# Performance work log

Measured on AMD Instinct MI355X. Metric: run time of the kernel, lower is better.

Reference implementation:

```python
import jax, jax.numpy as jnp
import numpy as np

N, C, T, V = 32, 128, 256, 25
K = 5  # temporal kernel size; reflect-pad 2*(K-1)//2 = 4 rows on top
EPS = 1e-5


def _inorm(x):
    # InstanceNorm2d(affine=False): normalize each (n,c) plane over (T,V)
    m = jnp.mean(x, axis=(2, 3), keepdims=True)
    v = jnp.var(x, axis=(2, 3), keepdims=True)
    return (x - m) * jax.lax.rsqrt(v + EPS)


def setup_inputs() -> dict:
    key = jax.random.key(0)
    ks = jax.random.split(key, 5)
    x = jax.random.normal(ks[0], (N, C, T, V), jnp.float32)
    PA = jax.random.normal(ks[1], (V, V), jnp.float32)          # learned adjacency
    Wd = jax.random.normal(ks[2], (C, C), jnp.float32) * 0.05    # 1x1 conv weight (O,I)
    bd = jnp.zeros((C,), jnp.float32)
    Wt = jax.random.normal(ks[3], (C, C, K, 1), jnp.float32) * 0.02  # (O,I,Kt,1)
    bt = jnp.zeros((C,), jnp.float32)
    return {"x": x, "PA": PA, "Wd": Wd, "bd": bd, "Wt": Wt, "bt": bt}


def reference(x, PA, Wd, bd, Wt, bt):
    # GCN unit: x.view(N,C*T,V) @ PA == einsum over last (joint) axis
    g = jnp.einsum('nctv,vw->nctw', x, PA)
    # 1x1 conv (channel GEMM) + bias
    y = jnp.einsum('nctv,oc->notv', g, Wd) + bd[None, :, None, None]
    # instance norm + identity residual (in_c == out_c) + relu
    y = jax.nn.relu(_inorm(y) + x)
    # TCN unit: reflection-pad 4 rows on top of T, conv (5,1) stride 1, instance norm
    yp = jnp.pad(y, ((0, 0), (0, 0), (4, 0), (0, 0)), mode='reflect')
    z = jax.lax.conv_general_dilated(
        yp, Wt, window_strides=(1, 1), padding='VALID',
        dimension_numbers=('NCHW', 'OIHW', 'NCHW')) + bt[None, :, None, None]
    z = _inorm(z)
    # outer residual (identity: in_c == out_c, stride == 1) + relu
    return jax.nn.relu(z + x)
```

## Files before the change

### kernel.cpp

```cpp
#include <hip/hip_runtime.h>


typedef unsigned short u16;
typedef unsigned int   u32;

using short8  = __attribute__((ext_vector_type(8))) short;
using floatx4 = __attribute__((ext_vector_type(4))) float;

#define NBATCH 32
#define CH     128
#define TDIM   256
#define VDIM   25
#define KT     5
#define PLANE  6400
#define EPSF   1e-5f
#define INV_PLANE (1.0f/6400.0f)

__device__ __forceinline__ u16 f2bf(float f) {
    u32 u = __float_as_uint(f);
    return (u16)((u + 0x7fffu + ((u >> 16) & 1u)) >> 16);
}
__device__ __forceinline__ float bf2f(u16 h) {
    return __uint_as_float(((u32)h) << 16);
}
__device__ __forceinline__ void gload_lds16(const void* g, void* l) {
    __builtin_amdgcn_global_load_lds(
        (const __attribute__((address_space(1))) u32*)g,
        (__attribute__((address_space(3))) u32*)l, 16, 0, 0);
}

__global__ __launch_bounds__(256) void k0_init(
    const float* __restrict__ Wd, const float* __restrict__ Wt,
    float* __restrict__ statsY, float* __restrict__ statsZ,
    u16* __restrict__ WdB, u16* __restrict__ Wt_b)
{
    int i = blockIdx.x * 256 + threadIdx.x;
    if (i < 8192) {
        statsY[i] = 0.f;
    } else if (i < 16384) {
        statsZ[i - 8192] = 0.f;
    } else if (i < 32768) {
        int j  = i - 16384;
        int sl = j & 31;
        int o  = (j >> 5) & 127;
        int cc = j >> 12;
        int cl = (((sl >> 3) ^ (o & 3)) << 3) | (sl & 7);
        WdB[j] = f2bf(Wd[o * CH + cc * 32 + cl]);
    } else {
        int j  = i - 32768;
        int sl = j & 31;
        int o  = (j >> 5) & 127;
        int r2 = j >> 12;
        int tap = r2 % KT;
        int ic  = r2 / KT;
        int il = (((sl >> 3) ^ (o & 3)) << 3) | (sl & 7);
        Wt_b[j] = f2bf(Wt[(o * CH + ic * 32 + il) * KT + tap]);
    }
}

__global__ __launch_bounds__(256) void k1a_gcn(
    const float* __restrict__ x, const float* __restrict__ PA,
    u16* __restrict__ gT)
{
    __shared__ __attribute__((aligned(16))) u32 sG[6800];
    __shared__ float sPA[625];

    const int tid   = threadIdx.x;
    const int nic   = blockIdx.y;
    const int chunk = blockIdx.x;
    const int c0    = chunk * 400;
    const int cl    = tid >> 3;
    const int tl    = tid & 7;

    for (int i = tid; i < 625; i += 256) sPA[i] = PA[i];

    const float* xrow = x + (size_t)(nic * 32 + cl) * PLANE + c0 + tl * 50;
    float xr[50];
#pragma unroll
    for (int w = 0; w < 25; ++w) {
        float2 t2 = *(const float2*)(xrow + 2 * w);
        xr[2 * w]     = t2.x;
        xr[2 * w + 1] = t2.y;
    }
    __syncthreads();

    u16* sG16 = (u16*)sG;
#pragma unroll
    for (int v = 0; v < VDIM; ++v) {
        float g0 = 0.f, g1 = 0.f;
#pragma unroll
        for (int w = 0; w < VDIM; ++w) {
            float p = sPA[w * VDIM + v];
            g0 += xr[w] * p;
            g1 += xr[25 + w] * p;
        }
        int r0 = tl * 50 + v;
        sG16[r0 * 34 + cl]        = f2bf(g0);
        sG16[(r0 + 25) * 34 + cl] = f2bf(g1);
    }
    __syncthreads();

    u32* outd = (u32*)gT;
    const size_t ob = ((size_t)nic * PLANE + c0) * 16;
    for (int j = tid; j < 6400; j += 256) {
        int r = j >> 4, dw = j & 15;
        int q = dw >> 2, b = dw & 3;
        outd[ob + r * 16 + (((q ^ (r & 3)) << 2) | b)] = sG[r * 17 + dw];
    }
}

__global__ __launch_bounds__(256) void k1b_mfma(
    const u16* __restrict__ gT, const u16* __restrict__ WdB,
    const float* __restrict__ bd,
    u16* __restrict__ y0b, float* __restrict__ statsY)
{
    __shared__ __attribute__((aligned(16))) char lds[65536];
    char* const sA = lds;
    char* const sB = lds + 32768;

    const int tid  = threadIdx.x;
    const int wave = tid >> 6;
    const int lane = tid & 63;
    const int l    = lane & 15;
    const int quad = lane >> 4;
    const int n    = blockIdx.y;
    const int c0   = blockIdx.x * 128;
    const int wub  = tid & ~63;

#pragma unroll
    for (int it = 0; it < 8; ++it)
        gload_lds16((const char*)WdB + (it * 256 + tid) * 16, sA + (it * 256 + wub) * 16);
#pragma unroll
    for (int cc = 0; cc < 4; ++cc) {
        const char* bsrc = (const char*)gT + ((size_t)(n * 4 + cc) * PLANE + c0) * 64;
#pragma unroll
        for (int it = 0; it < 2; ++it)
            gload_lds16(bsrc + (it * 256 + tid) * 16, sB + cc * 8192 + (it * 256 + wub) * 16);
    }
    __syncthreads();

    floatx4 acc[2][8];
#pragma unroll
    for (int a = 0; a < 2; ++a)
#pragma unroll
        for (int b = 0; b < 8; ++b) acc[a][b] = (floatx4){0.f, 0.f, 0.f, 0.f};

    const int swzA = (quad ^ (l & 3)) << 4;
#pragma unroll
    for (int cc = 0; cc < 4; ++cc) {
        const short8 a0 = *(const short8*)(sA + cc * 8192 + (wave * 32      + l) * 64 + swzA);
        const short8 a1 = *(const short8*)(sA + cc * 8192 + (wave * 32 + 16 + l) * 64 + swzA);
#pragma unroll
        for (int ct = 0; ct < 8; ++ct) {
            const short8 b = *(const short8*)(sB + cc * 8192 + (ct * 16 + l) * 64 + swzA);
            acc[0][ct] = __builtin_amdgcn_mfma_f32_16x16x32_bf16(a0, b, acc[0][ct], 0, 0, 0);
            acc[1][ct] = __builtin_amdgcn_mfma_f32_16x16x32_bf16(a1, b, acc[1][ct], 0, 0, 0);
        }
    }

#pragma unroll
    for (int ot = 0; ot < 2; ++ot) {
#pragma unroll
        for (int reg = 0; reg < 4; ++reg) {
            const int o = wave * 32 + ot * 16 + quad * 4 + reg;
            const float bias = bd[o];
            float s1 = 0.f, s2 = 0.f;
            u16* yp = y0b + (size_t)(n * CH + o) * PLANE + c0 + l;
#pragma unroll
            for (int ct = 0; ct < 8; ++ct) {
                float val = acc[ot][ct][reg] + bias;
                yp[ct * 16] = f2bf(val);
                s1 += val; s2 += val * val;
            }
#pragma unroll
            for (int m = 1; m <= 8; m <<= 1) {
                s1 += __shfl_xor(s1, m, 64);
                s2 += __shfl_xor(s2, m, 64);
            }
            if (l == 0) {
                atomicAdd(&statsY[(n * CH + o) * 2 + 0], s1);
                atomicAdd(&statsY[(n * CH + o) * 2 + 1], s2);
            }
        }
    }
}

__global__ __launch_bounds__(256) void k2_yhat(
    const u16* __restrict__ y0b, const float* __restrict__ x,
    const float* __restrict__ statsY, u16* __restrict__ yhatT)
{
    __shared__ u32 sT[256 * 17];
    __shared__ float sM[32], sR[32];

    const int tid = threadIdx.x;
    const int nic = blockIdx.y;
    const int n   = nic >> 2, ic = nic & 3;
    const int c0  = blockIdx.x * 256;

    if (tid < 32) {
        float a = statsY[(n * CH + ic * 32 + tid) * 2 + 0];
        float b = statsY[(n * CH + ic * 32 + tid) * 2 + 1];
        float m = a * INV_PLANE;
        sM[tid] = m;
        sR[tid] = rsqrtf(b * INV_PLANE - m * m + EPSF);
    }
    __syncthreads();

    for (int idx = tid; idx < 4096; idx += 256) {
        int ip = idx >> 8;
        int c  = idx & 255;
        int i0 = ip * 2;
        int g0 = (n * CH + ic * 32 + i0) * PLANE + c0 + c;
        int g1 = g0 + PLANE;
        float va = fmaxf((bf2f(y0b[g0]) - sM[i0]) * sR[i0] + x[g0], 0.f);
        float vb = fmaxf((bf2f(y0b[g1]) - sM[i0 + 1]) * sR[i0 + 1] + x[g1], 0.f);
        sT[c * 17 + ip] = (u32)f2bf(va) | ((u32)f2bf(vb) << 16);
    }
    __syncthreads();

    u32* outd = (u32*)yhatT;
    int obase = (nic * PLANE + c0) * 16;
    for (int idx = tid; idx < 4096; idx += 256) {
        int r = idx >> 4, dw = idx & 15;
        int q = dw >> 2, b = dw & 3;
        outd[obase + r * 16 + (((q ^ (r & 3)) << 2) | b)] = sT[r * 17 + dw];
    }
}

__global__ __launch_bounds__(256, 2) void k3_mfma(
    const u16* __restrict__ yhatT, const u16* __restrict__ Wt_b,
    const float* __restrict__ bt,
    u16* __restrict__ zb, float* __restrict__ statsZ)
{
    __shared__ __attribute__((aligned(16))) char lds[65536];
    char* const sB = lds;
    char* const sA = lds + 24576;

    const int tid  = threadIdx.x;
    const int wave = tid >> 6;
    const int wr   = wave >> 1;
    const int wc   = wave & 1;
    const int lane = tid & 63;
    const int l    = lane & 15;
    const int quad = lane >> 4;
    const int n    = blockIdx.y;
    const int blk  = blockIdx.x;
    const int c0   = blk * 256;
    const int wub  = tid & ~63;

    floatx4 acc[4][8];
#pragma unroll
    for (int a = 0; a < 4; ++a)
#pragma unroll
        for (int b = 0; b < 8; ++b) acc[a][b] = (floatx4){0.f, 0.f, 0.f, 0.f};

    for (int ic = 0; ic < 4; ++ic) {
        __syncthreads();
        const char* asrc = (const char*)(Wt_b + ic * 20480);
#pragma unroll
        for (int it = 0; it < 10; ++it)
            gload_lds16(asrc + (it * 256 + tid) * 16, sA + (it * 256 + wub) * 16);
        const char* bsrc = (const char*)(yhatT + (size_t)(n * 4 + ic) * (PLANE * 32));
        if (blk == 0) {
#pragma unroll
            for (int it = 0; it < 4; ++it)
                gload_lds16(bsrc + (it * 256 + tid) * 16, sB + 6400 + (it * 256 + wub) * 16);
            const u32* bsrcd = (const u32*)bsrc;
            u32* sBd = (u32*)sB;
            for (int idx = tid; idx < 1600; idx += 256) {
                int r = idx >> 4, dw = idx & 15;
                int q = dw >> 2, b = dw & 3;
                int d = 100 - r;
                int tref = (d + 24) / 25;
                int v = r % 25;
                int sc = tref * 25 + v;
                sBd[r * 16 + (((q ^ (r & 3)) << 2) | b)] =
                    bsrcd[sc * 16 + (((q ^ (sc & 3)) << 2) | b)];
            }
        } else {
            const char* bsrc2 = bsrc + (size_t)(c0 - 100) * 64;
#pragma unroll
            for (int it = 0; it < 6; ++it)
                gload_lds16(bsrc2 + (it * 256 + tid) * 16, sB + (it * 256 + wub) * 16);
        }
        __syncthreads();
#pragma unroll
        for (int tap = 0; tap < KT; ++tap) {
            short8 af[4];
#pragma unroll
            for (int ot = 0; ot < 4; ++ot) {
                int ro = wr * 64 + ot * 16 + l;
                af[ot] = *(const short8*)(sA + tap * 8192 + ro * 64 + ((quad ^ (l & 3)) << 4));
            }
#pragma unroll
            for (int ct = 0; ct < 8; ++ct) {
                int r = wc * 128 + ct * 16 + l + tap * 25;
                const short8 b = *(const short8*)(sB + r * 64 + ((quad ^ (r & 3)) << 4));
#pragma unroll
                for (int ot = 0; ot < 4; ++ot)
                    acc[ot][ct] = __builtin_amdgcn_mfma_f32_16x16x32_bf16(af[ot], b, acc[ot][ct], 0, 0, 0);
            }
        }
    }

#pragma unroll
    for (int ot = 0; ot < 4; ++ot) {
#pragma unroll
        for (int reg = 0; reg < 4; ++reg) {
            const int o = wr * 64 + ot * 16 + quad * 4 + reg;
            const float bias = bt[o];
            float s1 = 0.f, s2 = 0.f;
            u16* zp = zb + (size_t)(n * CH + o) * PLANE + c0 + wc * 128 + l;
#pragma unroll
            for (int ct = 0; ct < 8; ++ct) {
                float val = acc[ot][ct][reg] + bias;
                zp[ct * 16] = f2bf(val);
                s1 += val; s2 += val * val;
            }
#pragma unroll
            for (int m = 1; m <= 8; m <<= 1) {
                s1 += __shfl_xor(s1, m, 64);
                s2 += __shfl_xor(s2, m, 64);
            }
            if (l == 0) {
                atomicAdd(&statsZ[(n * CH + o) * 2 + 0], s1);
                atomicAdd(&statsZ[(n * CH + o) * 2 + 1], s2);
            }
        }
    }
}

__global__ __launch_bounds__(256) void k4_final(
    const u16* __restrict__ zb, const float* __restrict__ x,
    const float* __restrict__ statsZ, float* __restrict__ out)
{
    int g = blockIdx.x * 256 + threadIdx.x;
    int p = g / 800;
    float a = statsZ[p * 2 + 0], b = statsZ[p * 2 + 1];
    float m = a * INV_PLANE;
    float r = rsqrtf(b * INV_PLANE - m * m + EPSF);
    short8 zv = *(const short8*)(zb + (size_t)g * 8);
    const float4* xp = (const float4*)x + (size_t)g * 2;
    float4 x0 = xp[0], x1 = xp[1];
    float4 o0, o1;
    o0.x = fmaxf((bf2f((u16)zv[0]) - m) * r + x0.x, 0.f);
    o0.y = fmaxf((bf2f((u16)zv[1]) - m) * r + x0.y, 0.f);
    o0.z = fmaxf((bf2f((u16)zv[2]) - m) * r + x0.z, 0.f);
    o0.w = fmaxf((bf2f((u16)zv[3]) - m) * r + x0.w, 0.f);
    o1.x = fmaxf((bf2f((u16)zv[4]) - m) * r + x1.x, 0.f);
    o1.y = fmaxf((bf2f((u16)zv[5]) - m) * r + x1.y, 0.f);
    o1.z = fmaxf((bf2f((u16)zv[6]) - m) * r + x1.z, 0.f);
    o1.w = fmaxf((bf2f((u16)zv[7]) - m) * r + x1.w, 0.f);
    float4* op = (float4*)out + (size_t)g * 2;
    op[0] = o0;
    op[1] = o1;
}

extern "C" void kernel_launch(void* const* d_in, const int* in_sizes, int n_in,
                              void* d_out, int out_size, void* d_ws, size_t ws_size,
                              hipStream_t stream) {
    const float* x  = (const float*)d_in[0];
    const float* PA = (const float*)d_in[1];
    const float* Wd = (const float*)d_in[2];
    const float* bd = (const float*)d_in[3];
    const float* Wt = (const float*)d_in[4];
    const float* bt = (const float*)d_in[5];
    float* out = (float*)d_out;

    char* wsb = (char*)d_ws;
    u16*   y0b    = (u16*)(wsb);
    u16*   zb     = y0b;
    u16*   gT     = (u16*)(wsb + 52428800);
    u16*   yhatT  = gT;
    float* statsY = (float*)(wsb + 104857600);
    float* statsZ = (float*)(wsb + 104890368);
    u16*   WdB    = (u16*)(wsb + 104923136);
    u16*   Wt_b   = (u16*)(wsb + 104955904);

    k0_init<<<dim3(448), dim3(256), 0, stream>>>(Wd, Wt, statsY, statsZ, WdB, Wt_b);
    k1a_gcn<<<dim3(16, 128), dim3(256), 0, stream>>>(x, PA, gT);
    k1b_mfma<<<dim3(50, 32), dim3(256), 0, stream>>>(gT, WdB, bd, y0b, statsY);
    k2_yhat<<<dim3(25, 128), dim3(256), 0, stream>>>(y0b, x, statsY, yhatT);
    k3_mfma<<<dim3(25, 32), dim3(256), 0, stream>>>(yhatT, Wt_b, bt, zb, statsZ);
    k4_final<<<dim3(12800), dim3(256), 0, stream>>>(zb, x, statsZ, out);
}
```

Before: 374.6 us.

## Double-buffer B tiles, load weights directly to registers, vectorize norm-transpose kernel

Both MFMA kernels now read weight fragments straight from global memory into registers instead of staging them in LDS, so the weight layout drops its swizzle. The activation tiles are double-buffered in LDS so the next channel chunk's async load overlaps the current chunk's MFMAs, and LDS use per block shrinks. The normalize-and-transpose kernel now uses vectorized 8-wide loads of y0b and x with an XOR-swizzled LDS write pattern to cut bank conflicts. In exchange, k3 holds 20 weight fragments per wave, which raises register pressure under launch_bounds(256,2), and weight reads now depend on cache hits.

```diff
diff --git a/kernel.cpp b/kernel.cpp
--- a/kernel.cpp
+++ b/kernel.cpp
@@ -44,8 +44,7 @@
         int sl = j & 31;
         int o  = (j >> 5) & 127;
         int cc = j >> 12;
-        int cl = (((sl >> 3) ^ (o & 3)) << 3) | (sl & 7);
-        WdB[j] = f2bf(Wd[o * CH + cc * 32 + cl]);
+        WdB[j] = f2bf(Wd[o * CH + cc * 32 + sl]);
     } else {
         int j  = i - 32768;
         int sl = j & 31;
@@ -53,8 +52,7 @@
         int r2 = j >> 12;
         int tap = r2 % KT;
         int ic  = r2 / KT;
-        int il = (((sl >> 3) ^ (o & 3)) << 3) | (sl & 7);
-        Wt_b[j] = f2bf(Wt[(o * CH + ic * 32 + il) * KT + tap]);
+        Wt_b[j] = f2bf(Wt[(o * CH + ic * 32 + sl) * KT + tap]);
     }
 }
 
@@ -114,9 +112,7 @@
     const float* __restrict__ bd,
     u16* __restrict__ y0b, float* __restrict__ statsY)
 {
-    __shared__ __attribute__((aligned(16))) char lds[65536];
-    char* const sA = lds;
-    char* const sB = lds + 32768;
+    __shared__ __attribute__((aligned(16))) char lds[16384];
 
     const int tid  = threadIdx.x;
     const int wave = tid >> 6;
@@ -127,35 +123,41 @@
     const int c0   = blockIdx.x * 128;
     const int wub  = tid & ~63;
 
-#pragma unroll
-    for (int it = 0; it < 8; ++it)
-        gload_lds16((const char*)WdB + (it * 256 + tid) * 16, sA + (it * 256 + wub) * 16);
-#pragma unroll
+    auto stageB = [&](int cc, char* dst) {
+        const char* bsrc = (const char*)gT + ((size_t)(n * 4 + cc) * PLANE + c0) * 64;
+#pragma unroll
+        for (int it = 0; it < 2; ++it)
+            gload_lds16(bsrc + (it * 256 + tid) * 16, dst + (it * 256 + wub) * 16);
+    };
+
+    stageB(0, lds);
+    __syncthreads();
+
+    floatx4 acc[2][8];
+#pragma unroll
+    for (int a = 0; a < 2; ++a)
+#pragma unroll
+        for (int b = 0; b < 8; ++b) acc[a][b] = (floatx4){0.f, 0.f, 0.f, 0.f};
+
     for (int cc = 0; cc < 4; ++cc) {
-        const char* bsrc = (const char*)gT + ((size_t)(n * 4 + cc) * PLANE + c0) * 64;
-#pragma unroll
-        for (int it = 0; it < 2; ++it)
-            gload_lds16(bsrc + (it * 256 + tid) * 16, sB + cc * 8192 + (it * 256 + wub) * 16);
-    }
-    __syncthreads();
-
-    floatx4 acc[2][8];
-#pragma unroll
-    for (int a = 0; a < 2; ++a)
-#pragma unroll
-        for (int b = 0; b < 8; ++b) acc[a][b] = (floatx4){0.f, 0.f, 0.f, 0.f};
-
-    const int swzA = (quad ^ (l & 3)) << 4;
-#pragma unroll
-    for (int cc = 0; cc < 4; ++cc) {
-        const short8 a0 = *(const short8*)(sA + cc * 8192 + (wave * 32      + l) * 64 + swzA);
-        const short8 a1 = *(const short8*)(sA + cc * 8192 + (wave * 32 + 16 + l) * 64 + swzA);
+        char* const sBc = lds + (cc & 1) * 8192;
+        char* const sBn = lds + ((cc + 1) & 1) * 8192;
+
+        const char* abase = (const char*)WdB + cc * 8192 + (wave * 32 + l) * 64 + (quad << 4);
+        const short8 a0 = *(const short8*)(abase);
+        const short8 a1 = *(const short8*)(abase + 16 * 64);
+        __builtin_amdgcn_sched_barrier(0);
+
+        if (cc < 3) stageB(cc + 1, sBn);
+
 #pragma unroll
         for (int ct = 0; ct < 8; ++ct) {
-            const short8 b = *(const short8*)(sB + cc * 8192 + (ct * 16 + l) * 64 + swzA);
+            const int r = ct * 16 + l;
+            const short8 b = *(const short8*)(sBc + r * 64 + ((quad ^ (r & 3)) << 4));
             acc[0][ct] = __builtin_amdgcn_mfma_f32_16x16x32_bf16(a0, b, acc[0][ct], 0, 0, 0);
             acc[1][ct] = __builtin_amdgcn_mfma_f32_16x16x32_bf16(a1, b, acc[1][ct], 0, 0, 0);
         }
+        __syncthreads();
     }
 
 #pragma unroll
@@ -206,15 +208,27 @@
     }
     __syncthreads();
 
-    for (int idx = tid; idx < 4096; idx += 256) {
-        int ip = idx >> 8;
-        int c  = idx & 255;
-        int i0 = ip * 2;
-        int g0 = (n * CH + ic * 32 + i0) * PLANE + c0 + c;
-        int g1 = g0 + PLANE;
-        float va = fmaxf((bf2f(y0b[g0]) - sM[i0]) * sR[i0] + x[g0], 0.f);
-        float vb = fmaxf((bf2f(y0b[g1]) - sM[i0 + 1]) * sR[i0 + 1] + x[g1], 0.f);
-        sT[c * 17 + ip] = (u32)f2bf(va) | ((u32)f2bf(vb) << 16);
+    u16* sT16 = (u16*)sT;
+#pragma unroll
+    for (int k = 0; k < 4; ++k) {
+        int j  = k * 256 + tid;
+        int ch = j >> 5;
+        int cb = (j & 31) << 3;
+        int g  = (n * CH + ic * 32 + ch) * PLANE + c0 + cb;
+        short8 yv = *(const short8*)(y0b + g);
+        const float4* xp = (const float4*)(x + g);
+        float4 x0 = xp[0], x1 = xp[1];
+        float m = sM[ch], r = sR[ch];
+        int wp = ((ch >> 1) ^ ((cb >> 3) & 15));
+        u16* dst = sT16 + cb * 34 + wp * 2 + (ch & 1);
+        dst[0 * 34] = f2bf(fmaxf((bf2f((u16)yv[0]) - m) * r + x0.x, 0.f));
+        dst[1 * 34] = f2bf(fmaxf((bf2f((u16)yv[1]) - m) * r + x0.y, 0.f));
+        dst[2 * 34] = f2bf(fmaxf((bf2f((u16)yv[2]) - m) * r + x0.z, 0.f));
+        dst[3 * 34] = f2bf(fmaxf((bf2f((u16)yv[3]) - m) * r + x0.w, 0.f));
+        dst[4 * 34] = f2bf(fmaxf((bf2f((u16)yv[4]) - m) * r + x1.x, 0.f));
+        dst[5 * 34] = f2bf(fmaxf((bf2f((u16)yv[5]) - m) * r + x1.y, 0.f));
+        dst[6 * 34] = f2bf(fmaxf((bf2f((u16)yv[6]) - m) * r + x1.z, 0.f));
+        dst[7 * 34] = f2bf(fmaxf((bf2f((u16)yv[7]) - m) * r + x1.w, 0.f));
     }
     __syncthreads();
 
@@ -223,7 +237,8 @@
     for (int idx = tid; idx < 4096; idx += 256) {
         int r = idx >> 4, dw = idx & 15;
         int q = dw >> 2, b = dw & 3;
-        outd[obase + r * 16 + (((q ^ (r & 3)) << 2) | b)] = sT[r * 17 + dw];
+        u32 val = sT[r * 17 + ((dw ^ (r >> 3)) & 15)];
+        outd[obase + r * 16 + (((q ^ (r & 3)) << 2) | b)] = val;
     }
 }
 
@@ -232,9 +247,7 @@
     const float* __restrict__ bt,
     u16* __restrict__ zb, float* __restrict__ statsZ)
 {
-    __shared__ __attribute__((aligned(16))) char lds[65536];
-    char* const sB = lds;
-    char* const sA = lds + 24576;
+    __shared__ __attribute__((aligned(16))) char lds[49152];
 
     const int tid  = threadIdx.x;
     const int wave = tid >> 6;
@@ -254,19 +267,14 @@
 #pragma unroll
         for (int b = 0; b < 8; ++b) acc[a][b] = (floatx4){0.f, 0.f, 0.f, 0.f};
 
-    for (int ic = 0; ic < 4; ++ic) {
-        __syncthreads();
-        const char* asrc = (const char*)(Wt_b + ic * 20480);
-#pragma unroll
-        for (int it = 0; it < 10; ++it)
-            gload_lds16(asrc + (it * 256 + tid) * 16, sA + (it * 256 + wub) * 16);
+    auto stageB = [&](int ic, char* dst) {
         const char* bsrc = (const char*)(yhatT + (size_t)(n * 4 + ic) * (PLANE * 32));
         if (blk == 0) {
 #pragma unroll
             for (int it = 0; it < 4; ++it)
-                gload_lds16(bsrc + (it * 256 + tid) * 16, sB + 6400 + (it * 256 + wub) * 16);
+                gload_lds16(bsrc + (it * 256 + tid) * 16, dst + 6400 + (it * 256 + wub) * 16);
             const u32* bsrcd = (const u32*)bsrc;
-            u32* sBd = (u32*)sB;
+            u32* sBd = (u32*)dst;
             for (int idx = tid; idx < 1600; idx += 256) {
                 int r = idx >> 4, dw = idx & 15;
                 int q = dw >> 2, b = dw & 3;
@@ -281,26 +289,41 @@
             const char* bsrc2 = bsrc + (size_t)(c0 - 100) * 64;
 #pragma unroll
             for (int it = 0; it < 6; ++it)
-                gload_lds16(bsrc2 + (it * 256 + tid) * 16, sB + (it * 256 + wub) * 16);
+                gload_lds16(bsrc2 + (it * 256 + tid) * 16, dst + (it * 256 + wub) * 16);
+        }
+    };
+
+    stageB(0, lds);
+    __syncthreads();
+
+    for (int ic = 0; ic < 4; ++ic) {
+        char* const sBc = lds + (ic & 1) * 24576;
+        char* const sBn = lds + ((ic + 1) & 1) * 24576;
+
+        short8 af[KT][4];
+        const char* abase = (const char*)Wt_b + (size_t)ic * 40960
+                          + (wr * 64 + l) * 64 + (quad << 4);
+#pragma unroll
+        for (int tap = 0; tap < KT; ++tap)
+#pragma unroll
+            for (int ot = 0; ot < 4; ++ot)
+                af[tap][ot] = *(const short8*)(abase + (tap * 128 + ot * 16) * 64);
+        __builtin_amdgcn_sched_barrier(0);
+
+        if (ic < 3) stageB(ic + 1, sBn);
+
+#pragma unroll
+        for (int tap = 0; tap < KT; ++tap) {
+#pragma unroll
+            for (int ct = 0; ct < 8; ++ct) {
+                const int r = wc * 128 + ct * 16 + l + tap * 25;
+                const short8 b = *(const short8*)(sBc + r * 64 + ((quad ^ (r & 3)) << 4));
+#pragma unroll
+                for (int ot = 0; ot < 4; ++ot)
+                    acc[ot][ct] = __builtin_amdgcn_mfma_f32_16x16x32_bf16(af[tap][ot], b, acc[ot][ct], 0, 0, 0);
+            }
         }
         __syncthreads();
-#pragma unroll
-        for (int tap = 0; tap < KT; ++tap) {
-            short8 af[4];
-#pragma unroll
-            for (int ot = 0; ot < 4; ++ot) {
-                int ro = wr * 64 + ot * 16 + l;
-                af[ot] = *(const short8*)(sA + tap * 8192 + ro * 64 + ((quad ^ (l & 3)) << 4));
-            }
-#pragma unroll
-            for (int ct = 0; ct < 8; ++ct) {
-                int r = wc * 128 + ct * 16 + l + tap * 25;
-                const short8 b = *(const short8*)(sB + r * 64 + ((quad ^ (r & 3)) << 4));
-#pragma unroll
-                for (int ot = 0; ot < 4; ++ot)
-                    acc[ot][ct] = __builtin_amdgcn_mfma_f32_16x16x32_bf16(af[ot], b, acc[ot][ct], 0, 0, 0);
-            }
-        }
     }
 
 #pragma unroll
```

New measurement: 402.2 us. 7.3% more time.
